# Performance work log

Measured on AMD Instinct MI355X. Metric: run time of the kernel, lower is better.

Reference implementation:

```python
import jax, jax.numpy as jnp
import numpy as np

RANK = 8
ALPHA = 16.0
SCALING = ALPHA / RANK
EPS = 1e-8


def setup_inputs() -> dict:
    key = jax.random.key(0)
    k1, k2, k3, k4 = jax.random.split(key, 4)
    B, S, D_IN, D_OUT = 4, 2048, 4096, 4096
    x = jax.random.normal(k1, (B, S, D_IN), dtype=jnp.float32)
    base_output = jax.random.normal(k2, (B, S, D_OUT), dtype=jnp.float32)
    base_weight = jax.random.normal(k3, (D_OUT, D_IN), dtype=jnp.float32) * 0.02
    # orthogonal init for lora_A (rank x in_features)
    g = jax.random.normal(k4, (D_IN, RANK), dtype=jnp.float32)
    q, _ = jnp.linalg.qr(g)
    lora_A = q.T.astype(jnp.float32)  # [rank, in]
    # lora_B initialized to zeros in the module; use small random values so
    # the delta path is numerically exercised.
    lora_B = jax.random.normal(jax.random.fold_in(key, 5), (D_OUT, RANK), dtype=jnp.float32) * 0.01
    magnitude = jnp.ones((D_OUT,), dtype=jnp.float32)
    return {
        "x": x,
        "base_output": base_output,
        "base_weight": base_weight,
        "lora_A": lora_A,
        "lora_B": lora_B,
        "magnitude": magnitude,
    }


def reference(x, base_output, base_weight, lora_A, lora_B, magnitude):
    # Low-rank path: x @ A^T @ B^T, scaled.  (dropout p=0 -> identity)
    lora_x = jnp.einsum("bsi,ri->bsr", x, lora_A)            # [B,S,r]
    lora_out = jnp.einsum("bsr,or->bso", lora_x, lora_B)     # [B,S,out]
    delta_v = lora_out * SCALING
    # DoRA-style row norm of the updated weight (materializes full delta,
    # matching the original math exactly).
    updated_weight = base_weight + (lora_B @ lora_A) * SCALING  # [out,in]
    updated_norm = jnp.linalg.norm(updated_weight, axis=1) + EPS  # [out]
    mag_scale = magnitude / updated_norm                          # [out]
    output = (base_output + delta_v) * mag_scale[None, None, :]
    return output
```

## Files before the change

kernel.cpp:

```cpp
#include <hip/hip_runtime.h>
#include <math.h>

#define D_IN   4096
#define D_OUT  4096
#define M_ROWS 8192
#define RANK   8
#define SCALING 2.0f
#define EPS_N  1e-8f

typedef float f4_t __attribute__((ext_vector_type(4)));

__device__ __forceinline__ f4_t ntl4(const float* p) {
    return __builtin_nontemporal_load((const f4_t*)p);
}
__device__ __forceinline__ void nts4(float* p, f4_t v) {
    __builtin_nontemporal_store(v, (f4_t*)p);
}

__global__ __launch_bounds__(256, 2) void k_magscale(
    const float* __restrict__ W,
    const float* __restrict__ A,
    const float* __restrict__ Bl,
    const float* __restrict__ mag,
    float* __restrict__ mag_scale,
    float* __restrict__ Bm)
{
    const int wave = threadIdx.x >> 6;
    const int lane = threadIdx.x & 63;
    const int o0 = blockIdx.x * 8 + wave * 2;
    const float* W0 = W + (size_t)o0 * D_IN;
    const float* W1 = W0 + D_IN;

    float b0[RANK], b1[RANK];
#pragma unroll
    for (int r = 0; r < RANK; ++r) {
        b0[r] = Bl[o0 * RANK + r];
        b1[r] = Bl[(o0 + 1) * RANK + r];
    }

    float acc0 = 0.f, acc1 = 0.f;
    for (int i = lane * 4; i < D_IN; i += 256) {
        float4 a4[RANK];
#pragma unroll
        for (int r = 0; r < RANK; ++r)
            a4[r] = *(const float4*)(A + r * D_IN + i);
        f4_t w0 = ntl4(W0 + i);
        f4_t w1 = ntl4(W1 + i);

        float d0x = 0.f, d0y = 0.f, d0z = 0.f, d0w = 0.f;
        float d1x = 0.f, d1y = 0.f, d1z = 0.f, d1w = 0.f;
#pragma unroll
        for (int r = 0; r < RANK; ++r) {
            d0x += b0[r] * a4[r].x; d0y += b0[r] * a4[r].y;
            d0z += b0[r] * a4[r].z; d0w += b0[r] * a4[r].w;
            d1x += b1[r] * a4[r].x; d1y += b1[r] * a4[r].y;
            d1z += b1[r] * a4[r].z; d1w += b1[r] * a4[r].w;
        }
        float t;
        t = w0.x + SCALING * d0x; acc0 += t * t;
        t = w0.y + SCALING * d0y; acc0 += t * t;
        t = w0.z + SCALING * d0z; acc0 += t * t;
        t = w0.w + SCALING * d0w; acc0 += t * t;
        t = w1.x + SCALING * d1x; acc1 += t * t;
        t = w1.y + SCALING * d1y; acc1 += t * t;
        t = w1.z + SCALING * d1z; acc1 += t * t;
        t = w1.w + SCALING * d1w; acc1 += t * t;
    }
#pragma unroll
    for (int off = 32; off > 0; off >>= 1) {
        acc0 += __shfl_down(acc0, off, 64);
        acc1 += __shfl_down(acc1, off, 64);
    }
    if (lane == 0) {
        float ms0 = mag[o0] / (sqrtf(acc0) + EPS_N);
        float ms1 = mag[o0 + 1] / (sqrtf(acc1) + EPS_N);
        mag_scale[o0] = ms0;
        mag_scale[o0 + 1] = ms1;
#pragma unroll
        for (int r = 0; r < RANK; ++r) {
            Bm[o0 * RANK + r]       = SCALING * b0[r] * ms0;
            Bm[(o0 + 1) * RANK + r] = SCALING * b1[r] * ms1;
        }
    }
}

#define MT 16

__global__ __launch_bounds__(256, 2) void k_fused(
    const float* __restrict__ x,
    const float* __restrict__ A,
    const float* __restrict__ base,
    const float* __restrict__ Bm,
    const float* __restrict__ mag_scale,
    float* __restrict__ out)
{
    const int wave = threadIdx.x >> 6;
    const int lane = threadIdx.x & 63;
    const int mb = blockIdx.x * MT;

    __shared__ float slx[MT][RANK];

    const float* x0 = x + (size_t)(mb + wave * 4) * D_IN;
    float acc[4][RANK];
#pragma unroll
    for (int g = 0; g < 4; ++g)
#pragma unroll
        for (int r = 0; r < RANK; ++r) acc[g][r] = 0.f;

    for (int i = lane * 4; i < D_IN; i += 256) {
        float4 a4[RANK];
#pragma unroll
        for (int r = 0; r < RANK; ++r)
            a4[r] = *(const float4*)(A + r * D_IN + i);
#pragma unroll
        for (int g = 0; g < 4; ++g) {
            f4_t x4 = ntl4(x0 + (size_t)g * D_IN + i);
#pragma unroll
            for (int r = 0; r < RANK; ++r)
                acc[g][r] += x4.x * a4[r].x + x4.y * a4[r].y +
                             x4.z * a4[r].z + x4.w * a4[r].w;
        }
    }
#pragma unroll
    for (int g = 0; g < 4; ++g) {
#pragma unroll
        for (int r = 0; r < RANK; ++r) {
            float v = acc[g][r];
#pragma unroll
            for (int off = 32; off > 0; off >>= 1)
                v += __shfl_down(v, off, 64);
            if (lane == 0) slx[wave * 4 + g][r] = v;
        }
    }
    __syncthreads();

#pragma unroll
    for (int tile = 0; tile < 4; ++tile) {
        const int o = tile * 1024 + threadIdx.x * 4;
        const float4 ms4 = *(const float4*)(mag_scale + o);
        float bm[4][RANK];
#pragma unroll
        for (int j = 0; j < 4; ++j) {
            float4 lo = *(const float4*)(Bm + (size_t)(o + j) * RANK);
            float4 hi = *(const float4*)(Bm + (size_t)(o + j) * RANK + 4);
            bm[j][0] = lo.x; bm[j][1] = lo.y; bm[j][2] = lo.z; bm[j][3] = lo.w;
            bm[j][4] = hi.x; bm[j][5] = hi.y; bm[j][6] = hi.z; bm[j][7] = hi.w;
        }
        for (int mi = 0; mi < MT; ++mi) {
            const size_t row = (size_t)(mb + mi) * D_OUT + o;
            f4_t b4 = ntl4(base + row);
            float l[RANK];
#pragma unroll
            for (int r = 0; r < RANK; ++r) l[r] = slx[mi][r];

            float rx = b4.x * ms4.x;
            float ry = b4.y * ms4.y;
            float rz = b4.z * ms4.z;
            float rw = b4.w * ms4.w;
#pragma unroll
            for (int r = 0; r < RANK; ++r) {
                rx += l[r] * bm[0][r];
                ry += l[r] * bm[1][r];
                rz += l[r] * bm[2][r];
                rw += l[r] * bm[3][r];
            }
            f4_t res;
            res.x = rx; res.y = ry; res.z = rz; res.w = rw;
            nts4(out + row, res);
        }
    }
}

extern "C" void kernel_launch(void* const* d_in, const int* in_sizes, int n_in,
                              void* d_out, int out_size, void* d_ws, size_t ws_size,
                              hipStream_t stream) {
    const float* x        = (const float*)d_in[0];
    const float* base_out = (const float*)d_in[1];
    const float* base_w   = (const float*)d_in[2];
    const float* lora_A   = (const float*)d_in[3];
    const float* lora_B   = (const float*)d_in[4];
    const float* mag      = (const float*)d_in[5];
    float* out = (float*)d_out;

    float* mag_scale = (float*)d_ws;
    float* Bm        = mag_scale + D_OUT;

    k_magscale<<<D_OUT / 8, 256, 0, stream>>>(base_w, lora_A, lora_B, mag,
                                              mag_scale, Bm);
    k_fused<<<M_ROWS / MT, 256, 0, stream>>>(x, lora_A, base_out, Bm,
                                             mag_scale, out);
}
```

Before: 408.6 us.

## Merge row-norm and x·A^T into one pre-kernel and split the epilogue

Replaces the two-kernel schedule with a combined pre-pass that computes the weight row norms and the rank-8 projection lx = x·A^T in a single launch, so the two independent reductions share the GPU. A separate epilogue kernel then streams base_output in 32-row by 1024-column tiles with 8 loads in flight per thread. This targets the serialisation between the norm pass and the x reading, and the limited memory-level parallelism in the old fused epilogue. It costs an extra workspace buffer and a global round trip for lx, and falls back to the old path when the workspace is too small.

Measured after the change: 465.8 us. 1.14x slower.

```diff
diff --git a/kernel.cpp b/kernel.cpp
--- a/kernel.cpp
+++ b/kernel.cpp
@@ -17,13 +17,199 @@
     __builtin_nontemporal_store(v, (f4_t*)p);
 }
 
-__global__ __launch_bounds__(256, 2) void k_magscale(
+__global__ __launch_bounds__(256, 4) void k_pre(
     const float* __restrict__ W,
+    const float* __restrict__ x,
     const float* __restrict__ A,
     const float* __restrict__ Bl,
     const float* __restrict__ mag,
     float* __restrict__ mag_scale,
-    float* __restrict__ Bm)
+    float* __restrict__ Bm,
+    float* __restrict__ lx)
+{
+    const int t    = threadIdx.x;
+    const int wave = t >> 6;
+    const int lane = t & 63;
+
+    __shared__ float red[4][4][RANK];
+
+    if (blockIdx.x < 2048) {
+        const int o0 = blockIdx.x * 2;
+        const float* W0 = W + (size_t)o0 * D_IN;
+        const float* W1 = W0 + D_IN;
+
+        float b0[RANK], b1[RANK];
+#pragma unroll
+        for (int r = 0; r < RANK; ++r) {
+            b0[r] = Bl[o0 * RANK + r];
+            b1[r] = Bl[(o0 + 1) * RANK + r];
+        }
+
+        float acc0 = 0.f, acc1 = 0.f;
+#pragma unroll
+        for (int k = 0; k < 4; ++k) {
+            const int i = t * 4 + k * 1024;
+            f4_t w0 = ntl4(W0 + i);
+            f4_t w1 = ntl4(W1 + i);
+            float4 a4[RANK];
+#pragma unroll
+            for (int r = 0; r < RANK; ++r)
+                a4[r] = *(const float4*)(A + r * D_IN + i);
+
+            float d0x = 0.f, d0y = 0.f, d0z = 0.f, d0w = 0.f;
+            float d1x = 0.f, d1y = 0.f, d1z = 0.f, d1w = 0.f;
+#pragma unroll
+            for (int r = 0; r < RANK; ++r) {
+                d0x += b0[r] * a4[r].x; d0y += b0[r] * a4[r].y;
+                d0z += b0[r] * a4[r].z; d0w += b0[r] * a4[r].w;
+                d1x += b1[r] * a4[r].x; d1y += b1[r] * a4[r].y;
+                d1z += b1[r] * a4[r].z; d1w += b1[r] * a4[r].w;
+            }
+            float v;
+            v = w0.x + SCALING * d0x; acc0 += v * v;
+            v = w0.y + SCALING * d0y; acc0 += v * v;
+            v = w0.z + SCALING * d0z; acc0 += v * v;
+            v = w0.w + SCALING * d0w; acc0 += v * v;
+            v = w1.x + SCALING * d1x; acc1 += v * v;
+            v = w1.y + SCALING * d1y; acc1 += v * v;
+            v = w1.z + SCALING * d1z; acc1 += v * v;
+            v = w1.w + SCALING * d1w; acc1 += v * v;
+        }
+#pragma unroll
+        for (int off = 32; off > 0; off >>= 1) {
+            acc0 += __shfl_down(acc0, off, 64);
+            acc1 += __shfl_down(acc1, off, 64);
+        }
+        if (lane == 0) { red[wave][0][0] = acc0; red[wave][0][1] = acc1; }
+        __syncthreads();
+        if (t == 0) {
+            float s0 = red[0][0][0] + red[1][0][0] + red[2][0][0] + red[3][0][0];
+            float s1 = red[0][0][1] + red[1][0][1] + red[2][0][1] + red[3][0][1];
+            float ms0 = mag[o0]     / (sqrtf(s0) + EPS_N);
+            float ms1 = mag[o0 + 1] / (sqrtf(s1) + EPS_N);
+            mag_scale[o0]     = ms0;
+            mag_scale[o0 + 1] = ms1;
+            float4 v0, v1, v2, v3;
+            v0.x = SCALING * b0[0] * ms0; v0.y = SCALING * b0[1] * ms0;
+            v0.z = SCALING * b0[2] * ms0; v0.w = SCALING * b0[3] * ms0;
+            v1.x = SCALING * b0[4] * ms0; v1.y = SCALING * b0[5] * ms0;
+            v1.z = SCALING * b0[6] * ms0; v1.w = SCALING * b0[7] * ms0;
+            v2.x = SCALING * b1[0] * ms1; v2.y = SCALING * b1[1] * ms1;
+            v2.z = SCALING * b1[2] * ms1; v2.w = SCALING * b1[3] * ms1;
+            v3.x = SCALING * b1[4] * ms1; v3.y = SCALING * b1[5] * ms1;
+            v3.z = SCALING * b1[6] * ms1; v3.w = SCALING * b1[7] * ms1;
+            *(float4*)(Bm + (size_t)o0 * RANK)           = v0;
+            *(float4*)(Bm + (size_t)o0 * RANK + 4)       = v1;
+            *(float4*)(Bm + (size_t)(o0 + 1) * RANK)     = v2;
+            *(float4*)(Bm + (size_t)(o0 + 1) * RANK + 4) = v3;
+        }
+    } else {
+        const int m0 = (blockIdx.x - 2048) * 4;
+        const float* x0 = x + (size_t)m0 * D_IN;
+
+        float acc[4][RANK];
+#pragma unroll
+        for (int g = 0; g < 4; ++g)
+#pragma unroll
+            for (int r = 0; r < RANK; ++r) acc[g][r] = 0.f;
+
+#pragma unroll
+        for (int k = 0; k < 4; ++k) {
+            const int i = t * 4 + k * 1024;
+            float4 a4[RANK];
+#pragma unroll
+            for (int r = 0; r < RANK; ++r)
+                a4[r] = *(const float4*)(A + r * D_IN + i);
+#pragma unroll
+            for (int g = 0; g < 4; ++g) {
+                f4_t x4 = ntl4(x0 + (size_t)g * D_IN + i);
+#pragma unroll
+                for (int r = 0; r < RANK; ++r)
+                    acc[g][r] += x4.x * a4[r].x + x4.y * a4[r].y +
+                                 x4.z * a4[r].z + x4.w * a4[r].w;
+            }
+        }
+#pragma unroll
+        for (int g = 0; g < 4; ++g) {
+#pragma unroll
+            for (int r = 0; r < RANK; ++r) {
+                float v = acc[g][r];
+#pragma unroll
+                for (int off = 32; off > 0; off >>= 1)
+                    v += __shfl_down(v, off, 64);
+                if (lane == 0) red[wave][g][r] = v;
+            }
+        }
+        __syncthreads();
+        if (t < 32) {
+            const int g = t >> 3, r = t & 7;
+            float v = red[0][g][r] + red[1][g][r] + red[2][g][r] + red[3][g][r];
+            lx[(size_t)(m0 + g) * RANK + r] = v;
+        }
+    }
+}
+
+#define EMT 32
+
+__global__ __launch_bounds__(256, 4) void k_epi(
+    const float* __restrict__ base,
+    const float* __restrict__ lx,
+    const float* __restrict__ Bm,
+    const float* __restrict__ mag_scale,
+    float* __restrict__ out)
+{
+    const int t    = threadIdx.x;
+    const int mb   = (blockIdx.x >> 2) * EMT;
+    const int tile = blockIdx.x & 3;
+    const int o    = tile * 1024 + t * 4;
+
+    __shared__ float slx[EMT][RANK];
+    slx[t >> 3][t & 7] = lx[(size_t)(mb + (t >> 3)) * RANK + (t & 7)];
+
+    const float4 ms4 = *(const float4*)(mag_scale + o);
+    float bm[4][RANK];
+#pragma unroll
+    for (int j = 0; j < 4; ++j) {
+        float4 lo = *(const float4*)(Bm + (size_t)(o + j) * RANK);
+        float4 hi = *(const float4*)(Bm + (size_t)(o + j) * RANK + 4);
+        bm[j][0] = lo.x; bm[j][1] = lo.y; bm[j][2] = lo.z; bm[j][3] = lo.w;
+        bm[j][4] = hi.x; bm[j][5] = hi.y; bm[j][6] = hi.z; bm[j][7] = hi.w;
+    }
+    __syncthreads();
+
+    for (int mi0 = 0; mi0 < EMT; mi0 += 8) {
+        f4_t b4[8];
+#pragma unroll
+        for (int j = 0; j < 8; ++j)
+            b4[j] = ntl4(base + (size_t)(mb + mi0 + j) * D_OUT + o);
+#pragma unroll
+        for (int j = 0; j < 8; ++j) {
+            const int mi = mi0 + j;
+            float4 llo = *(const float4*)&slx[mi][0];
+            float4 lhi = *(const float4*)&slx[mi][4];
+            float l[RANK] = { llo.x, llo.y, llo.z, llo.w,
+                              lhi.x, lhi.y, lhi.z, lhi.w };
+            float rx = b4[j].x * ms4.x;
+            float ry = b4[j].y * ms4.y;
+            float rz = b4[j].z * ms4.z;
+            float rw = b4[j].w * ms4.w;
+#pragma unroll
+            for (int r = 0; r < RANK; ++r) {
+                rx += l[r] * bm[0][r];
+                ry += l[r] * bm[1][r];
+                rz += l[r] * bm[2][r];
+                rw += l[r] * bm[3][r];
+            }
+            f4_t res; res.x = rx; res.y = ry; res.z = rz; res.w = rw;
+            nts4(out + (size_t)(mb + mi) * D_OUT + o, res);
+        }
+    }
+}
+
+__global__ __launch_bounds__(256, 2) void k_magscale(
+    const float* __restrict__ W, const float* __restrict__ A,
+    const float* __restrict__ Bl, const float* __restrict__ mag,
+    float* __restrict__ mag_scale, float* __restrict__ Bm)
 {
     const int wave = threadIdx.x >> 6;
     const int lane = threadIdx.x & 63;
@@ -37,7 +223,6 @@
         b0[r] = Bl[o0 * RANK + r];
         b1[r] = Bl[(o0 + 1) * RANK + r];
     }
-
     float acc0 = 0.f, acc1 = 0.f;
     for (int i = lane * 4; i < D_IN; i += 256) {
         float4 a4[RANK];
@@ -46,7 +231,6 @@
             a4[r] = *(const float4*)(A + r * D_IN + i);
         f4_t w0 = ntl4(W0 + i);
         f4_t w1 = ntl4(W1 + i);
-
         float d0x = 0.f, d0y = 0.f, d0z = 0.f, d0w = 0.f;
         float d1x = 0.f, d1y = 0.f, d1z = 0.f, d1w = 0.f;
 #pragma unroll
@@ -56,15 +240,15 @@
             d1x += b1[r] * a4[r].x; d1y += b1[r] * a4[r].y;
             d1z += b1[r] * a4[r].z; d1w += b1[r] * a4[r].w;
         }
-        float t;
-        t = w0.x + SCALING * d0x; acc0 += t * t;
-        t = w0.y + SCALING * d0y; acc0 += t * t;
-        t = w0.z + SCALING * d0z; acc0 += t * t;
-        t = w0.w + SCALING * d0w; acc0 += t * t;
-        t = w1.x + SCALING * d1x; acc1 += t * t;
-        t = w1.y + SCALING * d1y; acc1 += t * t;
-        t = w1.z + SCALING * d1z; acc1 += t * t;
-        t = w1.w + SCALING * d1w; acc1 += t * t;
+        float v;
+        v = w0.x + SCALING * d0x; acc0 += v * v;
+        v = w0.y + SCALING * d0y; acc0 += v * v;
+        v = w0.z + SCALING * d0z; acc0 += v * v;
+        v = w0.w + SCALING * d0w; acc0 += v * v;
+        v = w1.x + SCALING * d1x; acc1 += v * v;
+        v = w1.y + SCALING * d1y; acc1 += v * v;
+        v = w1.z + SCALING * d1z; acc1 += v * v;
+        v = w1.w + SCALING * d1w; acc1 += v * v;
     }
 #pragma unroll
     for (int off = 32; off > 0; off >>= 1) {
@@ -85,19 +269,14 @@
 }
 
 #define MT 16
-
 __global__ __launch_bounds__(256, 2) void k_fused(
-    const float* __restrict__ x,
-    const float* __restrict__ A,
-    const float* __restrict__ base,
-    const float* __restrict__ Bm,
-    const float* __restrict__ mag_scale,
-    float* __restrict__ out)
+    const float* __restrict__ x, const float* __restrict__ A,
+    const float* __restrict__ base, const float* __restrict__ Bm,
+    const float* __restrict__ mag_scale, float* __restrict__ out)
 {
     const int wave = threadIdx.x >> 6;
     const int lane = threadIdx.x & 63;
     const int mb = blockIdx.x * MT;
-
     __shared__ float slx[MT][RANK];
 
     const float* x0 = x + (size_t)(mb + wave * 4) * D_IN;
@@ -152,7 +331,6 @@
             float l[RANK];
 #pragma unroll
             for (int r = 0; r < RANK; ++r) l[r] = slx[mi][r];
-
             float rx = b4.x * ms4.x;
             float ry = b4.y * ms4.y;
             float rz = b4.z * ms4.z;
@@ -164,8 +342,7 @@
                 rz += l[r] * bm[2][r];
                 rw += l[r] * bm[3][r];
             }
-            f4_t res;
-            res.x = rx; res.y = ry; res.z = rz; res.w = rw;
+            f4_t res; res.x = rx; res.y = ry; res.z = rz; res.w = rw;
             nts4(out + row, res);
         }
     }
@@ -184,9 +361,18 @@
 
     float* mag_scale = (float*)d_ws;
     float* Bm        = mag_scale + D_OUT;
-
-    k_magscale<<<D_OUT / 8, 256, 0, stream>>>(base_w, lora_A, lora_B, mag,
-                                              mag_scale, Bm);
-    k_fused<<<M_ROWS / MT, 256, 0, stream>>>(x, lora_A, base_out, Bm,
-                                             mag_scale, out);
-}
+    float* lx        = Bm + (size_t)D_OUT * RANK;
+
+    const size_t need = (size_t)(D_OUT + D_OUT * RANK + M_ROWS * RANK) * sizeof(float);
+    if (ws_size >= need) {
+        k_pre<<<4096, 256, 0, stream>>>(base_w, x, lora_A, lora_B, mag,
+                                        mag_scale, Bm, lx);
+        k_epi<<<(M_ROWS / EMT) * 4, 256, 0, stream>>>(base_out, lx, Bm,
+                                                      mag_scale, out);
+    } else {
+        k_magscale<<<D_OUT / 8, 256, 0, stream>>>(base_w, lora_A, lora_B, mag,
+                                                  mag_scale, Bm);
+        k_fused<<<M_ROWS / MT, 256, 0, stream>>>(x, lora_A, base_out, Bm,
+                                                 mag_scale, out);
+    }
+}
```
